# Optimization experiments

Measured on AMD Instinct MI355X. Metric: run time of the kernel, lower is better.

The kernel has to match this reference:

```python
import jax, jax.numpy as jnp
import numpy as np

N, E, H = 25000, 100000, 32          # nodes, edges, node/clique hidden dim
NC, A, EC = 8000, 50000, 24000       # cliques, node2clique assignments, clique edges
EEMB, CEE, L = 8, 8, 2               # edge emb dims, n layers


def segment_mean(vals, ids, num):
    s = jax.ops.segment_sum(vals, ids, num_segments=num)
    cnt = jax.ops.segment_sum(jnp.ones(ids.shape[0], vals.dtype), ids, num_segments=num)
    return s / jnp.maximum(cnt, 1.0)[:, None]


def setup_inputs() -> dict:
    key = jax.random.key(0)
    ks = jax.random.split(key, 24)
    s = 0.1  # param scale
    inp = {
        "node_features": jax.random.normal(ks[0], (N, H), jnp.float32),
        "edge_index": jax.random.randint(ks[1], (2, E), 0, N),
        "edge_features": jax.random.normal(ks[2], (E, EEMB), jnp.float32),
        "clique_features": jax.random.normal(ks[3], (NC, H), jnp.float32),
        "node2clique_index": jnp.stack([
            jax.random.randint(ks[4], (A,), 0, N),
            jax.random.randint(ks[5], (A,), 0, NC)]),
        "clique_edge_index": jax.random.randint(ks[6], (2, EC), 0, NC),
        "clique_edge_features": jax.random.normal(ks[7], (EC, CEE), jnp.float32),
        # node NNConv params (stacked over L layers)
        "nn1_w": jax.random.normal(ks[8], (L, EEMB, H)) * s,
        "nn1_b": jnp.zeros((L, H)),
        "nn2_w": jax.random.normal(ks[9], (L, H, H * H)) * s,
        "nn2_b": jnp.zeros((L, H * H)),
        "root_w": jax.random.normal(ks[10], (L, H, H)) * s,
        "root_b": jnp.zeros((L, H)),
        # Node2Clique linear
        "n2c_w": jax.random.normal(ks[11], (L, H, H)) * s,
        "n2c_b": jnp.zeros((L, H)),
        # clique NNConv params
        "cnn1_w": jax.random.normal(ks[12], (L, CEE, H)) * s,
        "cnn1_b": jnp.zeros((L, H)),
        "cnn2_w": jax.random.normal(ks[13], (L, H, H * H)) * s,
        "cnn2_b": jnp.zeros((L, H * H)),
        "croot_w": jax.random.normal(ks[14], (L, H, H)) * s,
        "croot_b": jnp.zeros((L, H)),
        # Clique2Node linear
        "c2n_w": jax.random.normal(ks[15], (L, H, H)) * s,
        "c2n_b": jnp.zeros((L, H)),
    }
    return inp


def nnconv(x, src, dst, edge_attr, w1, b1, w2, b2, rw, rb, n_out_nodes):
    # per-edge weight matrices from the edge MLP: [E, in, out]
    h = jax.nn.relu(edge_attr @ w1 + b1)
    We = (h @ w2 + b2).reshape(edge_attr.shape[0], x.shape[1], -1)
    msg = jnp.einsum('ei,eio->eo', x[src], We)           # message from source
    agg = segment_mean(msg, dst, n_out_nodes)            # mean aggregation at target
    return agg + x @ rw + rb                             # root weight + bias


def reference(node_features, edge_index, edge_features, clique_features,
              node2clique_index, clique_edge_index, clique_edge_features,
              nn1_w, nn1_b, nn2_w, nn2_b, root_w, root_b, n2c_w, n2c_b,
              cnn1_w, cnn1_b, cnn2_w, cnn2_b, croot_w, croot_b, c2n_w, c2n_b):
    x, c = node_features, clique_features
    src, dst = edge_index[0], edge_index[1]
    nid, cid = node2clique_index[0], node2clique_index[1]
    csrc, cdst = clique_edge_index[0], clique_edge_index[1]
    for l in range(L):
        # node-level edge-conditioned conv
        x = jax.nn.relu(nnconv(x, src, dst, edge_features,
                               nn1_w[l], nn1_b[l], nn2_w[l], nn2_b[l],
                               root_w[l], root_b[l], N))
        # Node2Clique: project node feats, scatter-mean into cliques
        m = x @ n2c_w[l] + n2c_b[l]
        c = c + segment_mean(m[nid], cid, NC)
        # clique-level edge-conditioned conv
        c = jax.nn.relu(nnconv(c, csrc, cdst, clique_edge_features,
                               cnn1_w[l], cnn1_b[l], cnn2_w[l], cnn2_b[l],
                               croot_w[l], croot_b[l], NC))
        # Clique2Node: project clique feats, scatter-mean back onto nodes
        m = c @ c2n_w[l] + c2n_b[l]
        x = x + segment_mean(m[cid], nid, N)
    return (x, c)
```

## Files before the change

### kernel.cpp

```cpp
#include <hip/hip_runtime.h>
#include <hip/hip_bf16.h>

typedef unsigned int u32;
typedef unsigned short u16;

#define DEVINL __device__ __forceinline__

constexpr int Nn  = 25000;
constexpr int Ee  = 100000;
constexpr int NCc = 8000;
constexpr int Aa  = 50000;
constexpr int ECc = 24000;
constexpr int TCOLS = 1088;
constexpr int WPSZ  = TCOLS*32;
constexpr int NSTR  = 580;
constexpr int NB_N = (Nn + 255)/256;
constexpr int NB_C = (NCc + 255)/256;

typedef float f32x4 __attribute__((ext_vector_type(4)));
typedef short s16x8 __attribute__((ext_vector_type(8)));

DEVINL float b2f(u16 u){ union{u32 i;float f;}v; v.i = ((u32)u)<<16; return v.f; }
DEVINL float bfl(u32 u){ union{u32 i;float f;}v; v.i = u<<16; return v.f; }
DEVINL float bfh(u32 u){ union{u32 i;float f;}v; v.i = u & 0xffff0000u; return v.f; }
DEVINL u16 f2b(float f){ union{float f;u32 i;}v; v.f=f; u32 i=v.i;
  return (u16)((i + 0x7fffu + ((i>>16)&1u)) >> 16); }
DEVINL u32 pk2(float a, float b){ return (u32)f2b(a) | ((u32)f2b(b) << 16); }
DEVINL float ldw(const void* p, long i, int f){
  return f ? ((const float*)p)[i] : b2f(((const u16*)p)[i]);
}

__global__ __launch_bounds__(256) void k_detect(const u16* __restrict__ p, int n,
                        u32* __restrict__ maxbits, int* __restrict__ zcnt,
                        int* __restrict__ done, int* __restrict__ flag){
  int i0 = blockIdx.x*256 + threadIdx.x;
  float lm = 0.f; int lz = 0;
  for (int i = i0; i < n; i += gridDim.x*256){
    u16 v = p[i];
    if (v == 0) lz++;
    lm = fmaxf(lm, fabsf(b2f(v)));
  }
  #pragma unroll
  for (int off = 32; off; off >>= 1){
    lm = fmaxf(lm, __shfl_down(lm, off));
    lz += __shfl_down(lz, off);
  }
  if ((threadIdx.x & 63) == 0){
    atomicMax(maxbits, __float_as_uint(lm));
    atomicAdd(zcnt, lz);
  }
  __syncthreads();
  if (threadIdx.x == 0){
    __threadfence();
    if (atomicAdd(done, 1) == gridDim.x - 1){
      float m = __uint_as_float(*maxbits);
      *flag = (m > 1e6f || *zcnt > n/4) ? 1 : 0;
    }
  }
}

__global__ __launch_bounds__(256) void k_conv_all(const void* __restrict__ xin, const void* __restrict__ cin,
                         float* __restrict__ xA, float* __restrict__ cA, const int* __restrict__ flag){
  int i = blockIdx.x*256 + threadIdx.x;
  int f = *flag;
  if (i < Nn*32) xA[i] = ldw(xin, i, f);
  else { i -= Nn*32; if (i < NCc*32) cA[i] = ldw(cin, i, f); }
}

__global__ __launch_bounds__(256) void k_count_all(const int* __restrict__ ei, const int* __restrict__ cei,
                          const int* __restrict__ n2c,
                          int* __restrict__ deg_nd, int* __restrict__ deg_ce,
                          int* __restrict__ deg_n2c, int* __restrict__ deg_c2n,
                          int* __restrict__ cnt_sn, int* __restrict__ cnt_sc){
  int i = blockIdx.x*256 + threadIdx.x;
  if (i < Ee)                             atomicAdd(&deg_nd[ei[Ee + i]], 1);
  else if ((i -= Ee) < ECc)               atomicAdd(&deg_ce[cei[ECc + i]], 1);
  else if ((i -= ECc) < Aa)               atomicAdd(&deg_n2c[n2c[Aa + i]], 1);
  else if ((i -= Aa) < Aa)                atomicAdd(&deg_c2n[n2c[i]], 1);
  else if ((i -= Aa) < Ee)                atomicAdd(&cnt_sn[ei[i]], 1);
  else if ((i -= Ee) < ECc)               atomicAdd(&cnt_sc[cei[i]], 1);
}

__global__ __launch_bounds__(256) void k_scan_block(
    const int* __restrict__ c0, const int* __restrict__ c1,
    const int* __restrict__ c2, const int* __restrict__ c3,
    int* __restrict__ o0, int* __restrict__ o1, int* __restrict__ o2, int* __restrict__ o3,
    int* __restrict__ b0, int* __restrict__ b1, int* __restrict__ b2, int* __restrict__ b3){
  __shared__ int s[256];
  int bid = blockIdx.x, seg, rb;
  if (bid < NB_N){ seg=0; rb=bid; }
  else if (bid < NB_N+NB_C){ seg=1; rb=bid-NB_N; }
  else if (bid < 2*NB_N+NB_C){ seg=2; rb=bid-NB_N-NB_C; }
  else { seg=3; rb=bid-2*NB_N-NB_C; }
  const int* cnt = seg==0?c0 : seg==1?c1 : seg==2?c2 : c3;
  int* offs = seg==0?o0 : seg==1?o1 : seg==2?o2 : o3;
  int* bs   = seg==0?b0 : seg==1?b1 : seg==2?b2 : b3;
  int M = (seg & 1) ? NCc : Nn;
  int tid = threadIdx.x;
  int i = rb*256 + tid;
  int v = (i < M) ? cnt[i] : 0;
  s[tid] = v; __syncthreads();
  for (int d = 1; d < 256; d <<= 1){
    int t = (tid >= d) ? s[tid-d] : 0;
    __syncthreads();
    s[tid] += t;
    __syncthreads();
  }
  if (i < M) offs[i] = s[tid] - v;
  if (tid == 255) bs[rb] = s[255];
}

__global__ __launch_bounds__(512) void k_spine(int* __restrict__ b0, int* __restrict__ b1,
                      int* __restrict__ b2, int* __restrict__ b3){
  __shared__ int s[512];
  int tid = threadIdx.x, seg = tid >> 7, lane = tid & 127;
  int NB = (seg & 1) ? NB_C : NB_N;
  int* bp = seg==0?b0 : seg==1?b1 : seg==2?b2 : b3;
  int v = (lane < NB) ? bp[lane] : 0;
  s[tid] = v; __syncthreads();
  for (int d = 1; d < 128; d <<= 1){
    int t = (lane >= d) ? s[tid-d] : 0;
    __syncthreads();
    s[tid] += t;
    __syncthreads();
  }
  if (lane < NB) bp[lane] = s[tid] - v;
}

__global__ __launch_bounds__(256) void k_scan_fix(
    int* __restrict__ o0, int* __restrict__ o1, int* __restrict__ o2, int* __restrict__ o3,
    const int* __restrict__ b0, const int* __restrict__ b1,
    const int* __restrict__ b2, const int* __restrict__ b3){
  int i = blockIdx.x*256 + threadIdx.x;
  if (i < Nn) o0[i] += b0[i >> 8];
  else if ((i -= Nn) < NCc) o1[i] += b1[i >> 8];
  else if ((i -= NCc) < Nn) o2[i] += b2[i >> 8];
  else if ((i -= Nn) < NCc) o3[i] += b3[i >> 8];
}

__global__ __launch_bounds__(256) void k_place(const int* __restrict__ ei, const int* __restrict__ cei,
                      const int* __restrict__ n2c,
                      const int* __restrict__ offs_n, const int* __restrict__ offs_c,
                      const int* __restrict__ offs_an, const int* __restrict__ offs_ac,
                      int* __restrict__ cur_n, int* __restrict__ cur_c,
                      int* __restrict__ cur_an, int* __restrict__ cur_ac,
                      int* __restrict__ perm_n, int* __restrict__ perm_c,
                      int* __restrict__ an2c, int* __restrict__ ac2n){
  int i = blockIdx.x*256 + threadIdx.x;
  if (i < Ee){
    int s = ei[i];
    perm_n[offs_n[s] + atomicAdd(&cur_n[s], 1)] = i;
  } else if ((i -= Ee) < ECc){
    int s = cei[i];
    perm_c[offs_c[s] + atomicAdd(&cur_c[s], 1)] = i;
  } else if ((i -= ECc) < Aa){
    int c = n2c[Aa + i];
    an2c[offs_ac[c] + atomicAdd(&cur_ac[c], 1)] = n2c[i];
  } else if ((i -= Aa) < Aa){
    int nd = n2c[i];
    ac2n[offs_an[nd] + atomicAdd(&cur_an[nd], 1)] = n2c[Aa + i];
  }
}

__global__ __launch_bounds__(256) void k_gather(const int* __restrict__ ei, const int* __restrict__ cei,
                       const int* __restrict__ perm_n, const int* __restrict__ perm_c,
                       const void* __restrict__ ef, const void* __restrict__ cef,
                       const int* __restrict__ flag,
                       int2* __restrict__ sdp_n, float* __restrict__ efp_n,
                       int2* __restrict__ sdp_c, float* __restrict__ efp_c){
  int i = blockIdx.x*256 + threadIdx.x;
  int f = *flag;
  if (i < Ee*8){
    int p = i >> 3, j = i & 7;
    int e = perm_n[p];
    efp_n[i] = ldw(ef, (long)e*8 + j, f);
    if (j == 0) sdp_n[p] = make_int2(ei[e], ei[Ee + e]);
  } else if ((i -= Ee*8) < ECc*8){
    int p = i >> 3, j = i & 7;
    int e = perm_c[p];
    efp_c[i] = ldw(cef, (long)e*8 + j, f);
    if (j == 0) sdp_c[p] = make_int2(cei[e], cei[ECc + e]);
  }
}

__global__ __launch_bounds__(256) void k_wpack_all(const void* __restrict__ nn2w, const void* __restrict__ nn2b,
                          const void* __restrict__ rootw,
                          const void* __restrict__ cnn2w, const void* __restrict__ cnn2b,
                          const void* __restrict__ crootw,
                          const int* __restrict__ flag, u16* __restrict__ Wp4){
  int i = blockIdx.x*256 + threadIdx.x;
  if (i >= 4*WPSZ) return;
  int set = i / WPSZ, j = i - set*WPSZ;
  int l = set >> 1, isC = set & 1;
  const void* W2 = isC ? cnn2w : nn2w;
  const void* B2 = isC ? cnn2b : nn2b;
  const void* RW = isC ? crootw : rootw;
  int f = *flag;
  int col = j >> 5, ii = j & 31;
  float v;
  if (col < 1024)      v = ldw(W2, (long)l*32768 + ((col>>5)<<10) + (ii<<5) + (col&31), f);
  else if (col < 1056) v = ldw(B2, (long)l*1024 + (ii<<5) + (col-1024), f);
  else                 v = ldw(RW, (long)l*1024 + (ii<<5) + (col-1056), f);
  Wp4[i] = f2b(v);
}

__global__ __launch_bounds__(512) void k_conv_fused(const float* __restrict__ base, int M,
                           const int2* __restrict__ sdp, const float* __restrict__ efp,
                           const int* __restrict__ offs, int E_,
                           const void* __restrict__ w1, long w1off,
                           const void* __restrict__ b1, long b1off,
                           const u16* __restrict__ Wp,
                           const void* __restrict__ rb, long rboff,
                           const int* __restrict__ flag,
                           float* __restrict__ feat_root, float* __restrict__ agg){
  __shared__ __align__(16) u32 Ts[16*NSTR];
  __shared__ float w1s[256];
  __shared__ __align__(8) u32 hws[8][4][16];
  int tid = threadIdx.x;
  int w = tid >> 6, lane = tid & 63;
  int quad = lane >> 4, lm = lane & 15;
  int n0 = blockIdx.x * 16;
  int f = *flag;
  if (tid < 256) w1s[tid] = ldw(w1, w1off + tid, f);
  float bb0 = ldw(b1, b1off + 2*lm, f);
  float bb1 = ldw(b1, b1off + 2*lm + 1, f);
  int n = n0 + lm;
  int nc = n < M ? n : M-1;
  const float* bp = base + (size_t)nc*32 + quad*8;
  s16x8 bfrag;
  #pragma unroll
  for (int j = 0; j < 8; j++) bfrag[j] = (short)f2b(bp[j]);
  #pragma unroll 1
  for (int ti = 0; ti < 9; ti++){
    int ct = w*9 + ti;
    if (ct >= 68) break;
    int colbase = ct*16;
    s16x8 afrag = *(const s16x8*)(Wp + (size_t)(colbase + lm)*32 + quad*8);
    f32x4 acc = {0.f, 0.f, 0.f, 0.f};
    acc = __builtin_amdgcn_mfma_f32_16x16x32_bf16(afrag, bfrag, acc, 0, 0, 0);
    if (ct < 66){
      int k = ct >> 1;
      int p0 = (ct & 1)*8 + quad*2;
      int idx = lm*NSTR + p0*36 + k;
      Ts[idx]      = pk2(acc[0], acc[1]);
      Ts[idx + 36] = pk2(acc[2], acc[3]);
    } else if (n < M){
      int o = (ct - 66)*16 + quad*4 - 0;
      o = (colbase + quad*4) - 1056;
      float4 v = make_float4(acc[0] + ldw(rb, rboff+o,   f),
                             acc[1] + ldw(rb, rboff+o+1, f),
                             acc[2] + ldw(rb, rboff+o+2, f),
                             acc[3] + ldw(rb, rboff+o+3, f));
      *(float4*)&feat_root[(size_t)n*32 + o] = v;
    }
  }
  __syncthreads();
  int lo = offs[n0];
  int hi = (n0 + 16 < M) ? offs[n0 + 16] : E_;
  int eg = quad, kk = lm;
  int pos = lo + w*4;
  float ef0 = 0.f, ef1 = 0.f; int sd0 = 0, sd1 = 0;
  if (lane < 32){
    int idx = pos*8 + lane;        if (idx < hi*8) ef0 = efp[idx];
    idx = (pos+32)*8 + lane;       if (idx < hi*8) ef1 = efp[idx];
  } else if (lane < 40){
    int idx = pos*2 + (lane-32);   if (idx < hi*2) sd0 = ((const int*)sdp)[idx];
    idx = (pos+32)*2 + (lane-32);  if (idx < hi*2) sd1 = ((const int*)sdp)[idx];
  }
  for (; pos < hi; pos += 32){
    int np = pos + 64;
    float ef2 = 0.f; int sd2 = 0;
    if (lane < 32){ int idx = np*8 + lane; if (idx < hi*8) ef2 = efp[idx]; }
    else if (lane < 40){ int idx = np*2 + (lane-32); if (idx < hi*2) sd2 = ((const int*)sdp)[idx]; }
    int sn = __shfl(sd0, 32 + 2*eg);
    int dn = __shfl(sd0, 33 + 2*eg);
    bool valid = (pos + eg < hi);
    int sr = sn - n0; sr = sr < 0 ? 0 : (sr > 15 ? 15 : sr);
    float a0 = bb0, a1 = bb1;
    #pragma unroll
    for (int j = 0; j < 8; j++){
      float ev = __shfl(ef0, eg*8 + j);
      a0 += ev * w1s[j*32 + 2*kk];
      a1 += ev * w1s[j*32 + 2*kk+1];
    }
    hws[w][eg][kk] = pk2(fmaxf(a0, 0.f), fmaxf(a1, 0.f));
    if (valid){
      const u32* Tr = &Ts[sr*NSTR + kk*36];
      u32 vb = Tr[32];
      float m0 = bfl(vb), m1 = bfh(vb);
      #pragma unroll
      for (int g = 0; g < 8; g++){
        uint4 tv = *(const uint4*)&Tr[g*4];
        uint2 hp = *(const uint2*)&hws[w][eg][g*2];
        float h0 = bfl(hp.x), h1 = bfh(hp.x), h2 = bfl(hp.y), h3 = bfh(hp.y);
        m0 += h0*bfl(tv.x) + h1*bfl(tv.y) + h2*bfl(tv.z) + h3*bfl(tv.w);
        m1 += h0*bfh(tv.x) + h1*bfh(tv.y) + h2*bfh(tv.z) + h3*bfh(tv.w);
      }
      float* ap = agg + (size_t)dn*32 + 2*kk;
      atomicAdd(ap,   m0);
      atomicAdd(ap+1, m1);
    }
    ef0 = ef1; sd0 = sd1; ef1 = ef2; sd1 = sd2;
  }
}

__global__ __launch_bounds__(256) void k_update_lin(const float* __restrict__ agg, const int* __restrict__ deg,
                           const float* __restrict__ feat_root, int M,
                           const void* __restrict__ w, long woff,
                           const void* __restrict__ b, long boff,
                           const int* __restrict__ flag,
                           float* __restrict__ feat, void* __restrict__ dt_out, long dt_off,
                           float* __restrict__ m_out){
  __shared__ float wsm[1024], bs[32], rows[8][33];
  int tid = threadIdx.x;
  int f = *flag;
  for (int idx = tid; idx < 1024; idx += 256) wsm[idx] = ldw(w, woff + idx, f);
  if (tid < 32) bs[tid] = ldw(b, boff + tid, f);
  int nl = tid >> 5, o = tid & 31;
  int n = blockIdx.x*8 + nl;
  long i = (long)n*32 + o;
  if (n < M){
    int dg = deg[n];
    float d = (float)(dg > 1 ? dg : 1);
    float v = fmaxf(agg[i]/d + feat_root[i], 0.f);
    rows[nl][o] = v;
    if (feat) feat[i] = v;
    if (dt_out){
      if (f) ((float*)dt_out)[dt_off + i] = v;
      else   ((u16*)dt_out)[dt_off + i]   = f2b(v);
    }
  }
  __syncthreads();
  if (n >= M) return;
  float acc = bs[o];
  #pragma unroll
  for (int j = 0; j < 32; j++) acc += rows[nl][j]*wsm[j*32+o];
  m_out[i] = acc;
}

__global__ __launch_bounds__(256) void k_segmean(const float* __restrict__ base, const float* __restrict__ m,
                        const int* __restrict__ idxarr, const int* __restrict__ offs,
                        const int* __restrict__ deg, int M, float* __restrict__ out){
  int i = blockIdx.x*256 + threadIdx.x;
  if (i >= M*32) return;
  int c = i >> 5, o = i & 31;
  int lo = offs[c], cnt = deg[c];
  float s = 0.f;
  for (int a = lo; a < lo + cnt; a++) s += m[(size_t)idxarr[a]*32 + o];
  out[i] = base[i] + s/(float)(cnt > 1 ? cnt : 1);
}

__global__ __launch_bounds__(256) void k_segmean_out(const float* __restrict__ base, const float* __restrict__ m,
                        const int* __restrict__ idxarr, const int* __restrict__ offs,
                        const int* __restrict__ deg, int M,
                        void* __restrict__ out, const int* __restrict__ flag){
  int i = blockIdx.x*256 + threadIdx.x;
  if (i >= M*32) return;
  int c = i >> 5, o = i & 31;
  int lo = offs[c], cnt = deg[c];
  float s = 0.f;
  for (int a = lo; a < lo + cnt; a++) s += m[(size_t)idxarr[a]*32 + o];
  float v = base[i] + s/(float)(cnt > 1 ? cnt : 1);
  if (*flag) ((float*)out)[i] = v;
  else       ((u16*)out)[i]   = f2b(v);
}

extern "C" void kernel_launch(void* const* d_in, const int* in_sizes, int n_in,
                              void* d_out, int out_size, void* d_ws, size_t ws_size,
                              hipStream_t stream){
  const int* ei  = (const int*)d_in[1];
  const int* n2c = (const int*)d_in[4];
  const int* cei = (const int*)d_in[5];
  const void *efr = d_in[2], *cefr = d_in[6];
  const void *nn1w = d_in[7], *nn1b = d_in[8], *nn2w = d_in[9], *nn2b = d_in[10],
             *rootw = d_in[11], *rootb = d_in[12], *n2cw = d_in[13], *n2cb = d_in[14],
             *cnn1w = d_in[15], *cnn1b = d_in[16], *cnn2w = d_in[17], *cnn2b = d_in[18],
             *crootw = d_in[19], *crootb = d_in[20], *c2nw = d_in[21], *c2nb = d_in[22];

  char* ws = (char*)d_ws;
  size_t off = 0;
  auto alloc = [&](size_t bytes){ void* p = ws + off; off += (bytes + 255) & ~(size_t)255; return p; };

  size_t zstart = off;
  float* aggE0  = (float*)alloc((size_t)Nn*32*4);
  float* aggE1  = (float*)alloc((size_t)Nn*32*4);
  float* caggE0 = (float*)alloc((size_t)NCc*32*4);
  float* caggE1 = (float*)alloc((size_t)NCc*32*4);
  int* deg_nd  = (int*)alloc((size_t)Nn*4);
  int* deg_ce  = (int*)alloc((size_t)NCc*4);
  int* deg_n2c = (int*)alloc((size_t)NCc*4);
  int* deg_c2n = (int*)alloc((size_t)Nn*4);
  int* cnt_sn  = (int*)alloc((size_t)Nn*4);
  int* cnt_sc  = (int*)alloc((size_t)NCc*4);
  int* cur_n   = (int*)alloc((size_t)Nn*4);
  int* cur_c   = (int*)alloc((size_t)NCc*4);
  int* cur_an  = (int*)alloc((size_t)Nn*4);
  int* cur_ac  = (int*)alloc((size_t)NCc*4);
  u32* maxbits = (u32*)alloc(256);
  int* zcnt = (int*)((char*)maxbits + 4);
  int* flag = (int*)((char*)maxbits + 8);
  int* done = (int*)((char*)maxbits + 12);
  size_t zbytes = off - zstart;

  float* xA  = (float*)alloc((size_t)Nn*32*4);
  float* xB  = (float*)alloc((size_t)Nn*32*4);
  float* xA1 = (float*)alloc((size_t)Nn*32*4);
  float* xC  = (float*)alloc((size_t)Nn*32*4);
  float* cA  = (float*)alloc((size_t)NCc*32*4);
  float* cB  = (float*)alloc((size_t)NCc*32*4);
  float* cC0 = (float*)alloc((size_t)NCc*32*4);
  float* cB1 = (float*)alloc((size_t)NCc*32*4);
  float* m_n = (float*)alloc((size_t)Nn*32*4);
  float* m_c = (float*)alloc((size_t)NCc*32*4);
  float* frn = (float*)alloc((size_t)Nn*32*4);
  float* frc = (float*)alloc((size_t)NCc*32*4);
  int* offs_n  = (int*)alloc((size_t)Nn*4);
  int* offs_c  = (int*)alloc((size_t)NCc*4);
  int* offs_an = (int*)alloc((size_t)Nn*4);
  int* offs_ac = (int*)alloc((size_t)NCc*4);
  int* bsum0 = (int*)alloc(512);
  int* bsum1 = (int*)alloc(512);
  int* bsum2 = (int*)alloc(512);
  int* bsum3 = (int*)alloc(512);
  int* perm_n = (int*)alloc((size_t)Ee*4);
  int* perm_c = (int*)alloc((size_t)ECc*4);
  int* an2c = (int*)alloc((size_t)Aa*4);
  int* ac2n = (int*)alloc((size_t)Aa*4);
  int2* sdp_n = (int2*)alloc((size_t)Ee*8);
  int2* sdp_c = (int2*)alloc((size_t)ECc*8);
  float* efp_n = (float*)alloc((size_t)Ee*8*4);
  float* efp_c = (float*)alloc((size_t)ECc*8*4);
  u16* Wp4 = (u16*)alloc((size_t)4*WPSZ*2);

  auto nb = [](int n){ return (n + 255)/256; };

  hipMemsetAsync(ws + zstart, 0, zbytes, stream);
  k_detect<<<256,256,0,stream>>>((const u16*)d_in[0], Nn*32, maxbits, zcnt, done, flag);
  k_conv_all<<<nb(Nn*32 + NCc*32),256,0,stream>>>(d_in[0], d_in[3], xA, cA, flag);
  k_count_all<<<nb(2*Ee + 2*ECc + 2*Aa),256,0,stream>>>(ei, cei, n2c,
      deg_nd, deg_ce, deg_n2c, deg_c2n, cnt_sn, cnt_sc);
  k_scan_block<<<2*(NB_N+NB_C),256,0,stream>>>(cnt_sn, cnt_sc, deg_c2n, deg_n2c,
      offs_n, offs_c, offs_an, offs_ac, bsum0, bsum1, bsum2, bsum3);
  k_spine<<<1,512,0,stream>>>(bsum0, bsum1, bsum2, bsum3);
  k_scan_fix<<<nb(2*(Nn+NCc)),256,0,stream>>>(offs_n, offs_c, offs_an, offs_ac,
      bsum0, bsum1, bsum2, bsum3);
  k_place<<<nb(Ee+ECc+2*Aa),256,0,stream>>>(ei, cei, n2c, offs_n, offs_c, offs_an, offs_ac,
      cur_n, cur_c, cur_an, cur_ac, perm_n, perm_c, an2c, ac2n);
  k_gather<<<nb(8*(Ee+ECc)),256,0,stream>>>(ei, cei, perm_n, perm_c, efr, cefr, flag,
      sdp_n, efp_n, sdp_c, efp_c);
  k_wpack_all<<<nb(4*WPSZ),256,0,stream>>>(nn2w, nn2b, rootw, cnn2w, cnn2b, crootw, flag, Wp4);

  int Gn = (Nn + 15)/16, Gc = (NCc + 15)/16;

  k_conv_fused<<<Gn,512,0,stream>>>(xA, Nn, sdp_n, efp_n, offs_n, Ee,
      nn1w, 0, nn1b, 0, Wp4 + 0*WPSZ, rootb, 0, flag, frn, aggE0);
  k_update_lin<<<(Nn+7)/8,256,0,stream>>>(aggE0, deg_nd, frn, Nn, n2cw, 0, n2cb, 0, flag,
      xB, nullptr, 0, m_n);
  k_segmean<<<nb(NCc*32),256,0,stream>>>(cA, m_n, an2c, offs_ac, deg_n2c, NCc, cB);
  k_conv_fused<<<Gc,512,0,stream>>>(cB, NCc, sdp_c, efp_c, offs_c, ECc,
      cnn1w, 0, cnn1b, 0, Wp4 + 1*WPSZ, crootb, 0, flag, frc, caggE0);
  k_update_lin<<<(NCc+7)/8,256,0,stream>>>(caggE0, deg_ce, frc, NCc, c2nw, 0, c2nb, 0, flag,
      cC0, nullptr, 0, m_c);
  k_segmean<<<nb(Nn*32),256,0,stream>>>(xB, m_c, ac2n, offs_an, deg_c2n, Nn, xA1);
  k_conv_fused<<<Gn,512,0,stream>>>(xA1, Nn, sdp_n, efp_n, offs_n, Ee,
      nn1w, 256, nn1b, 32, Wp4 + 2*WPSZ, rootb, 32, flag, frn, aggE1);
  k_update_lin<<<(Nn+7)/8,256,0,stream>>>(aggE1, deg_nd, frn, Nn, n2cw, 1024, n2cb, 32, flag,
      xC, nullptr, 0, m_n);
  k_segmean<<<nb(NCc*32),256,0,stream>>>(cC0, m_n, an2c, offs_ac, deg_n2c, NCc, cB1);
  k_conv_fused<<<Gc,512,0,stream>>>(cB1, NCc, sdp_c, efp_c, offs_c, ECc,
      cnn1w, 256, cnn1b, 32, Wp4 + 3*WPSZ, crootb, 32, flag, frc, caggE1);
  k_update_lin<<<(NCc+7)/8,256,0,stream>>>(caggE1, deg_ce, frc, NCc, c2nw, 1024, c2nb, 32, flag,
      nullptr, d_out, (long)Nn*32, m_c);
  k_segmean_out<<<nb(Nn*32),256,0,stream>>>(xC, m_c, ac2n, offs_an, deg_c2n, Nn, d_out, flag);
}
```

Measured before the change: 351.1 us.

## Replace atomic edge aggregation with dst-CSR message buffer and fuse segment-mean into conv

The edge conv no longer does float atomicAdds into a per-node aggregate. Each edge writes its bf16-packed message into a slot ordered by destination node, using a new destination CSR built in the existing scan/place kernels. The update kernel then reduces each node's messages deterministically. The separate segment-mean kernels are folded into the conv kernel's input load, removing launches and intermediate buffers. In exchange it adds bf16 rounding of messages, an extra message buffer round-trip, and redundant per-quad segment gathers inside the conv.

```diff
diff --git a/kernel.cpp b/kernel.cpp
--- a/kernel.cpp
+++ b/kernel.cpp
@@ -82,22 +82,25 @@
 }
 
 __global__ __launch_bounds__(256) void k_scan_block(
-    const int* __restrict__ c0, const int* __restrict__ c1,
-    const int* __restrict__ c2, const int* __restrict__ c3,
-    int* __restrict__ o0, int* __restrict__ o1, int* __restrict__ o2, int* __restrict__ o3,
-    int* __restrict__ b0, int* __restrict__ b1, int* __restrict__ b2, int* __restrict__ b3){
+    const int* __restrict__ c0, const int* __restrict__ c1, const int* __restrict__ c2,
+    const int* __restrict__ c3, const int* __restrict__ c4, const int* __restrict__ c5,
+    int* __restrict__ o0, int* __restrict__ o1, int* __restrict__ o2,
+    int* __restrict__ o3, int* __restrict__ o4, int* __restrict__ o5,
+    int* __restrict__ b0, int* __restrict__ b1, int* __restrict__ b2,
+    int* __restrict__ b3, int* __restrict__ b4, int* __restrict__ b5){
   __shared__ int s[256];
-  int bid = blockIdx.x, seg, rb;
-  if (bid < NB_N){ seg=0; rb=bid; }
-  else if (bid < NB_N+NB_C){ seg=1; rb=bid-NB_N; }
-  else if (bid < 2*NB_N+NB_C){ seg=2; rb=bid-NB_N-NB_C; }
-  else { seg=3; rb=bid-2*NB_N-NB_C; }
-  const int* cnt = seg==0?c0 : seg==1?c1 : seg==2?c2 : c3;
-  int* offs = seg==0?o0 : seg==1?o1 : seg==2?o2 : o3;
-  int* bs   = seg==0?b0 : seg==1?b1 : seg==2?b2 : b3;
+  int bid = blockIdx.x, seg = 0;
+  for (;;){
+    int nb = (seg & 1) ? NB_C : NB_N;
+    if (bid < nb) break;
+    bid -= nb; seg++;
+  }
+  const int* cnt = seg==0?c0 : seg==1?c1 : seg==2?c2 : seg==3?c3 : seg==4?c4 : c5;
+  int* offs = seg==0?o0 : seg==1?o1 : seg==2?o2 : seg==3?o3 : seg==4?o4 : o5;
+  int* bs   = seg==0?b0 : seg==1?b1 : seg==2?b2 : seg==3?b3 : seg==4?b4 : b5;
   int M = (seg & 1) ? NCc : Nn;
   int tid = threadIdx.x;
-  int i = rb*256 + tid;
+  int i = bid*256 + tid;
   int v = (i < M) ? cnt[i] : 0;
   s[tid] = v; __syncthreads();
   for (int d = 1; d < 256; d <<= 1){
@@ -107,15 +110,16 @@
     __syncthreads();
   }
   if (i < M) offs[i] = s[tid] - v;
-  if (tid == 255) bs[rb] = s[255];
-}
-
-__global__ __launch_bounds__(512) void k_spine(int* __restrict__ b0, int* __restrict__ b1,
-                      int* __restrict__ b2, int* __restrict__ b3){
-  __shared__ int s[512];
+  if (tid == 255) bs[bid] = s[255];
+}
+
+__global__ __launch_bounds__(768) void k_spine(int* __restrict__ b0, int* __restrict__ b1,
+                      int* __restrict__ b2, int* __restrict__ b3,
+                      int* __restrict__ b4, int* __restrict__ b5){
+  __shared__ int s[768];
   int tid = threadIdx.x, seg = tid >> 7, lane = tid & 127;
   int NB = (seg & 1) ? NB_C : NB_N;
-  int* bp = seg==0?b0 : seg==1?b1 : seg==2?b2 : b3;
+  int* bp = seg==0?b0 : seg==1?b1 : seg==2?b2 : seg==3?b3 : seg==4?b4 : b5;
   int v = (lane < NB) ? bp[lane] : 0;
   s[tid] = v; __syncthreads();
   for (int d = 1; d < 128; d <<= 1){
@@ -128,31 +132,41 @@
 }
 
 __global__ __launch_bounds__(256) void k_scan_fix(
-    int* __restrict__ o0, int* __restrict__ o1, int* __restrict__ o2, int* __restrict__ o3,
-    const int* __restrict__ b0, const int* __restrict__ b1,
-    const int* __restrict__ b2, const int* __restrict__ b3){
+    int* __restrict__ o0, int* __restrict__ o1, int* __restrict__ o2,
+    int* __restrict__ o3, int* __restrict__ o4, int* __restrict__ o5,
+    const int* __restrict__ b0, const int* __restrict__ b1, const int* __restrict__ b2,
+    const int* __restrict__ b3, const int* __restrict__ b4, const int* __restrict__ b5){
   int i = blockIdx.x*256 + threadIdx.x;
   if (i < Nn) o0[i] += b0[i >> 8];
   else if ((i -= Nn) < NCc) o1[i] += b1[i >> 8];
   else if ((i -= NCc) < Nn) o2[i] += b2[i >> 8];
   else if ((i -= Nn) < NCc) o3[i] += b3[i >> 8];
+  else if ((i -= NCc) < Nn) o4[i] += b4[i >> 8];
+  else if ((i -= Nn) < NCc) o5[i] += b5[i >> 8];
 }
 
 __global__ __launch_bounds__(256) void k_place(const int* __restrict__ ei, const int* __restrict__ cei,
                       const int* __restrict__ n2c,
                       const int* __restrict__ offs_n, const int* __restrict__ offs_c,
                       const int* __restrict__ offs_an, const int* __restrict__ offs_ac,
+                      const int* __restrict__ doffs_n, const int* __restrict__ doffs_c,
                       int* __restrict__ cur_n, int* __restrict__ cur_c,
                       int* __restrict__ cur_an, int* __restrict__ cur_ac,
+                      int* __restrict__ curd_n, int* __restrict__ curd_c,
                       int* __restrict__ perm_n, int* __restrict__ perm_c,
+                      int* __restrict__ dq_n, int* __restrict__ dq_c,
                       int* __restrict__ an2c, int* __restrict__ ac2n){
   int i = blockIdx.x*256 + threadIdx.x;
   if (i < Ee){
-    int s = ei[i];
-    perm_n[offs_n[s] + atomicAdd(&cur_n[s], 1)] = i;
+    int s = ei[i], d = ei[Ee + i];
+    int p = offs_n[s] + atomicAdd(&cur_n[s], 1);
+    int q = doffs_n[d] + atomicAdd(&curd_n[d], 1);
+    perm_n[p] = i; dq_n[p] = q;
   } else if ((i -= Ee) < ECc){
-    int s = cei[i];
-    perm_c[offs_c[s] + atomicAdd(&cur_c[s], 1)] = i;
+    int s = cei[i], d = cei[ECc + i];
+    int p = offs_c[s] + atomicAdd(&cur_c[s], 1);
+    int q = doffs_c[d] + atomicAdd(&curd_c[d], 1);
+    perm_c[p] = i; dq_c[p] = q;
   } else if ((i -= ECc) < Aa){
     int c = n2c[Aa + i];
     an2c[offs_ac[c] + atomicAdd(&cur_ac[c], 1)] = n2c[i];
@@ -164,6 +178,7 @@
 
 __global__ __launch_bounds__(256) void k_gather(const int* __restrict__ ei, const int* __restrict__ cei,
                        const int* __restrict__ perm_n, const int* __restrict__ perm_c,
+                       const int* __restrict__ dq_n, const int* __restrict__ dq_c,
                        const void* __restrict__ ef, const void* __restrict__ cef,
                        const int* __restrict__ flag,
                        int2* __restrict__ sdp_n, float* __restrict__ efp_n,
@@ -174,12 +189,12 @@
     int p = i >> 3, j = i & 7;
     int e = perm_n[p];
     efp_n[i] = ldw(ef, (long)e*8 + j, f);
-    if (j == 0) sdp_n[p] = make_int2(ei[e], ei[Ee + e]);
+    if (j == 0) sdp_n[p] = make_int2(ei[e], dq_n[p]);
   } else if ((i -= Ee*8) < ECc*8){
     int p = i >> 3, j = i & 7;
     int e = perm_c[p];
     efp_c[i] = ldw(cef, (long)e*8 + j, f);
-    if (j == 0) sdp_c[p] = make_int2(cei[e], cei[ECc + e]);
+    if (j == 0) sdp_c[p] = make_int2(cei[e], dq_c[p]);
   }
 }
 
@@ -204,7 +219,9 @@
   Wp4[i] = f2b(v);
 }
 
-__global__ __launch_bounds__(512) void k_conv_fused(const float* __restrict__ base, int M,
+__global__ __launch_bounds__(512) void k_conv_fused(const float* __restrict__ base,
+                           const float* __restrict__ mprev, const int* __restrict__ aidx,
+                           const int* __restrict__ aoffs, const int* __restrict__ adeg, int M,
                            const int2* __restrict__ sdp, const float* __restrict__ efp,
                            const int* __restrict__ offs, int E_,
                            const void* __restrict__ w1, long w1off,
@@ -212,7 +229,7 @@
                            const u16* __restrict__ Wp,
                            const void* __restrict__ rb, long rboff,
                            const int* __restrict__ flag,
-                           float* __restrict__ feat_root, float* __restrict__ agg){
+                           float* __restrict__ feat_root, u32* __restrict__ msg){
   __shared__ __align__(16) u32 Ts[16*NSTR];
   __shared__ float w1s[256];
   __shared__ __align__(8) u32 hws[8][4][16];
@@ -227,9 +244,24 @@
   int n = n0 + lm;
   int nc = n < M ? n : M-1;
   const float* bp = base + (size_t)nc*32 + quad*8;
+  float fv[8];
+  #pragma unroll
+  for (int j = 0; j < 8; j++) fv[j] = bp[j];
+  if (aidx){
+    int lo = aoffs[nc], cnt = adeg[nc];
+    float sacc[8] = {0,0,0,0,0,0,0,0};
+    for (int a = lo; a < lo + cnt; a++){
+      const float* mp = mprev + (size_t)aidx[a]*32 + quad*8;
+      #pragma unroll
+      for (int j = 0; j < 8; j++) sacc[j] += mp[j];
+    }
+    float inv = 1.f/(float)(cnt > 1 ? cnt : 1);
+    #pragma unroll
+    for (int j = 0; j < 8; j++) fv[j] += sacc[j]*inv;
+  }
   s16x8 bfrag;
   #pragma unroll
-  for (int j = 0; j < 8; j++) bfrag[j] = (short)f2b(bp[j]);
+  for (int j = 0; j < 8; j++) bfrag[j] = (short)f2b(fv[j]);
   #pragma unroll 1
   for (int ti = 0; ti < 9; ti++){
     int ct = w*9 + ti;
@@ -245,8 +277,7 @@
       Ts[idx]      = pk2(acc[0], acc[1]);
       Ts[idx + 36] = pk2(acc[2], acc[3]);
     } else if (n < M){
-      int o = (ct - 66)*16 + quad*4 - 0;
-      o = (colbase + quad*4) - 1056;
+      int o = (colbase + quad*4) - 1056;
       float4 v = make_float4(acc[0] + ldw(rb, rboff+o,   f),
                              acc[1] + ldw(rb, rboff+o+1, f),
                              acc[2] + ldw(rb, rboff+o+2, f),
@@ -273,7 +304,7 @@
     if (lane < 32){ int idx = np*8 + lane; if (idx < hi*8) ef2 = efp[idx]; }
     else if (lane < 40){ int idx = np*2 + (lane-32); if (idx < hi*2) sd2 = ((const int*)sdp)[idx]; }
     int sn = __shfl(sd0, 32 + 2*eg);
-    int dn = __shfl(sd0, 33 + 2*eg);
+    int dq = __shfl(sd0, 33 + 2*eg);
     bool valid = (pos + eg < hi);
     int sr = sn - n0; sr = sr < 0 ? 0 : (sr > 15 ? 15 : sr);
     float a0 = bb0, a1 = bb1;
@@ -296,15 +327,14 @@
         m0 += h0*bfl(tv.x) + h1*bfl(tv.y) + h2*bfl(tv.z) + h3*bfl(tv.w);
         m1 += h0*bfh(tv.x) + h1*bfh(tv.y) + h2*bfh(tv.z) + h3*bfh(tv.w);
       }
-      float* ap = agg + (size_t)dn*32 + 2*kk;
-      atomicAdd(ap,   m0);
-      atomicAdd(ap+1, m1);
+      msg[(size_t)dq*16 + kk] = pk2(m0, m1);
     }
     ef0 = ef1; sd0 = sd1; ef1 = ef2; sd1 = sd2;
   }
 }
 
-__global__ __launch_bounds__(256) void k_update_lin(const float* __restrict__ agg, const int* __restrict__ deg,
+__global__ __launch_bounds__(256) void k_update_lin(const u32* __restrict__ msg,
+                           const int* __restrict__ doffs, const int* __restrict__ ddeg,
                            const float* __restrict__ feat_root, int M,
                            const void* __restrict__ w, long woff,
                            const void* __restrict__ b, long boff,
@@ -320,9 +350,11 @@
   int n = blockIdx.x*8 + nl;
   long i = (long)n*32 + o;
   if (n < M){
-    int dg = deg[n];
-    float d = (float)(dg > 1 ? dg : 1);
-    float v = fmaxf(agg[i]/d + feat_root[i], 0.f);
+    int lo = doffs[n], cnt = ddeg[n];
+    const u16* mp = (const u16*)msg;
+    float s = 0.f;
+    for (int a = 0; a < cnt; a++) s += b2f(mp[(size_t)(lo+a)*32 + o]);
+    float v = fmaxf(s/(float)(cnt > 1 ? cnt : 1) + feat_root[i], 0.f);
     rows[nl][o] = v;
     if (feat) feat[i] = v;
     if (dt_out){
@@ -336,18 +368,6 @@
   #pragma unroll
   for (int j = 0; j < 32; j++) acc += rows[nl][j]*wsm[j*32+o];
   m_out[i] = acc;
-}
-
-__global__ __launch_bounds__(256) void k_segmean(const float* __restrict__ base, const float* __restrict__ m,
-                        const int* __restrict__ idxarr, const int* __restrict__ offs,
-                        const int* __restrict__ deg, int M, float* __restrict__ out){
-  int i = blockIdx.x*256 + threadIdx.x;
-  if (i >= M*32) return;
-  int c = i >> 5, o = i & 31;
-  int lo = offs[c], cnt = deg[c];
-  float s = 0.f;
-  for (int a = lo; a < lo + cnt; a++) s += m[(size_t)idxarr[a]*32 + o];
-  out[i] = base[i] + s/(float)(cnt > 1 ? cnt : 1);
 }
 
 __global__ __launch_bounds__(256) void k_segmean_out(const float* __restrict__ base, const float* __restrict__ m,
@@ -382,10 +402,6 @@
   auto alloc = [&](size_t bytes){ void* p = ws + off; off += (bytes + 255) & ~(size_t)255; return p; };
 
   size_t zstart = off;
-  float* aggE0  = (float*)alloc((size_t)Nn*32*4);
-  float* aggE1  = (float*)alloc((size_t)Nn*32*4);
-  float* caggE0 = (float*)alloc((size_t)NCc*32*4);
-  float* caggE1 = (float*)alloc((size_t)NCc*32*4);
   int* deg_nd  = (int*)alloc((size_t)Nn*4);
   int* deg_ce  = (int*)alloc((size_t)NCc*4);
   int* deg_n2c = (int*)alloc((size_t)NCc*4);
@@ -396,6 +412,8 @@
   int* cur_c   = (int*)alloc((size_t)NCc*4);
   int* cur_an  = (int*)alloc((size_t)Nn*4);
   int* cur_ac  = (int*)alloc((size_t)NCc*4);
+  int* curd_n  = (int*)alloc((size_t)Nn*4);
+  int* curd_c  = (int*)alloc((size_t)NCc*4);
   u32* maxbits = (u32*)alloc(256);
   int* zcnt = (int*)((char*)maxbits + 4);
   int* flag = (int*)((char*)maxbits + 8);
@@ -404,12 +422,9 @@
 
   float* xA  = (float*)alloc((size_t)Nn*32*4);
   float* xB  = (float*)alloc((size_t)Nn*32*4);
-  float* xA1 = (float*)alloc((size_t)Nn*32*4);
   float* xC  = (float*)alloc((size_t)Nn*32*4);
   float* cA  = (float*)alloc((size_t)NCc*32*4);
-  float* cB  = (float*)alloc((size_t)NCc*32*4);
   float* cC0 = (float*)alloc((size_t)NCc*32*4);
-  float* cB1 = (float*)alloc((size_t)NCc*32*4);
   float* m_n = (float*)alloc((size_t)Nn*32*4);
   float* m_c = (float*)alloc((size_t)NCc*32*4);
   float* frn = (float*)alloc((size_t)Nn*32*4);
@@ -418,18 +433,23 @@
   int* offs_c  = (int*)alloc((size_t)NCc*4);
   int* offs_an = (int*)alloc((size_t)Nn*4);
   int* offs_ac = (int*)alloc((size_t)NCc*4);
-  int* bsum0 = (int*)alloc(512);
-  int* bsum1 = (int*)alloc(512);
-  int* bsum2 = (int*)alloc(512);
-  int* bsum3 = (int*)alloc(512);
+  int* doffs_n = (int*)alloc((size_t)Nn*4);
+  int* doffs_c = (int*)alloc((size_t)NCc*4);
+  int* bs0 = (int*)alloc(512); int* bs1 = (int*)alloc(512);
+  int* bs2 = (int*)alloc(512); int* bs3 = (int*)alloc(512);
+  int* bs4 = (int*)alloc(512); int* bs5 = (int*)alloc(512);
   int* perm_n = (int*)alloc((size_t)Ee*4);
   int* perm_c = (int*)alloc((size_t)ECc*4);
+  int* dq_n = (int*)alloc((size_t)Ee*4);
+  int* dq_c = (int*)alloc((size_t)ECc*4);
   int* an2c = (int*)alloc((size_t)Aa*4);
   int* ac2n = (int*)alloc((size_t)Aa*4);
   int2* sdp_n = (int2*)alloc((size_t)Ee*8);
   int2* sdp_c = (int2*)alloc((size_t)ECc*8);
   float* efp_n = (float*)alloc((size_t)Ee*8*4);
   float* efp_c = (float*)alloc((size_t)ECc*8*4);
+  u32* msg_n = (u32*)alloc((size_t)Ee*16*4);
+  u32* msg_c = (u32*)alloc((size_t)ECc*16*4);
   u16* Wp4 = (u16*)alloc((size_t)4*WPSZ*2);
 
   auto nb = [](int n){ return (n + 255)/256; };
@@ -439,37 +459,35 @@
   k_conv_all<<<nb(Nn*32 + NCc*32),256,0,stream>>>(d_in[0], d_in[3], xA, cA, flag);
   k_count_all<<<nb(2*Ee + 2*ECc + 2*Aa),256,0,stream>>>(ei, cei, n2c,
       deg_nd, deg_ce, deg_n2c, deg_c2n, cnt_sn, cnt_sc);
-  k_scan_block<<<2*(NB_N+NB_C),256,0,stream>>>(cnt_sn, cnt_sc, deg_c2n, deg_n2c,
-      offs_n, offs_c, offs_an, offs_ac, bsum0, bsum1, bsum2, bsum3);
-  k_spine<<<1,512,0,stream>>>(bsum0, bsum1, bsum2, bsum3);
-  k_scan_fix<<<nb(2*(Nn+NCc)),256,0,stream>>>(offs_n, offs_c, offs_an, offs_ac,
-      bsum0, bsum1, bsum2, bsum3);
+  k_scan_block<<<3*(NB_N+NB_C),256,0,stream>>>(cnt_sn, cnt_sc, deg_c2n, deg_n2c, deg_nd, deg_ce,
+      offs_n, offs_c, offs_an, offs_ac, doffs_n, doffs_c, bs0, bs1, bs2, bs3, bs4, bs5);
+  k_spine<<<1,768,0,stream>>>(bs0, bs1, bs2, bs3, bs4, bs5);
+  k_scan_fix<<<nb(3*(Nn+NCc)),256,0,stream>>>(offs_n, offs_c, offs_an, offs_ac, doffs_n, doffs_c,
+      bs0, bs1, bs2, bs3, bs4, bs5);
   k_place<<<nb(Ee+ECc+2*Aa),256,0,stream>>>(ei, cei, n2c, offs_n, offs_c, offs_an, offs_ac,
-      cur_n, cur_c, cur_an, cur_ac, perm_n, perm_c, an2c, ac2n);
-  k_gather<<<nb(8*(Ee+ECc)),256,0,stream>>>(ei, cei, perm_n, perm_c, efr, cefr, flag,
+      doffs_n, doffs_c, cur_n, cur_c, cur_an, cur_ac, curd_n, curd_c,
+      perm_n, perm_c, dq_n, dq_c, an2c, ac2n);
+  k_gather<<<nb(8*(Ee+ECc)),256,0,stream>>>(ei, cei, perm_n, perm_c, dq_n, dq_c, efr, cefr, flag,
       sdp_n, efp_n, sdp_c, efp_c);
   k_wpack_all<<<nb(4*WPSZ),256,0,stream>>>(nn2w, nn2b, rootw, cnn2w, cnn2b, crootw, flag, Wp4);
 
   int Gn = (Nn + 15)/16, Gc = (NCc + 15)/16;
 
-  k_conv_fused<<<Gn,512,0,stream>>>(xA, Nn, sdp_n, efp_n, offs_n, Ee,
-      nn1w, 0, nn1b, 0, Wp4 + 0*WPSZ, rootb, 0, flag, frn, aggE0);
-  k_update_lin<<<(Nn+7)/8,256,0,stream>>>(aggE0, deg_nd, frn, Nn, n2cw, 0, n2cb, 0, flag,
-      xB, nullptr, 0, m_n);
-  k_segmean<<<nb(NCc*32),256,0,stream>>>(cA, m_n, an2c, offs_ac, deg_n2c, NCc, cB);
-  k_conv_fused<<<Gc,512,0,stream>>>(cB, NCc, sdp_c, efp_c, offs_c, ECc,
-      cnn1w, 0, cnn1b, 0, Wp4 + 1*WPSZ, crootb, 0, flag, frc, caggE0);
-  k_update_lin<<<(NCc+7)/8,256,0,stream>>>(caggE0, deg_ce, frc, NCc, c2nw, 0, c2nb, 0, flag,
-      cC0, nullptr, 0, m_c);
-  k_segmean<<<nb(Nn*32),256,0,stream>>>(xB, m_c, ac2n, offs_an, deg_c2n, Nn, xA1);
-  k_conv_fused<<<Gn,512,0,stream>>>(xA1, Nn, sdp_n, efp_n, offs_n, Ee,
-      nn1w, 256, nn1b, 32, Wp4 + 2*WPSZ, rootb, 32, flag, frn, aggE1);
-  k_update_lin<<<(Nn+7)/8,256,0,stream>>>(aggE1, deg_nd, frn, Nn, n2cw, 1024, n2cb, 32, flag,
-      xC, nullptr, 0, m_n);
-  k_segmean<<<nb(NCc*32),256,0,stream>>>(cC0, m_n, an2c, offs_ac, deg_n2c, NCc, cB1);
-  k_conv_fused<<<Gc,512,0,stream>>>(cB1, NCc, sdp_c, efp_c, offs_c, ECc,
-      cnn1w, 256, cnn1b, 32, Wp4 + 3*WPSZ, crootb, 32, flag, frc, caggE1);
-  k_update_lin<<<(NCc+7)/8,256,0,stream>>>(caggE1, deg_ce, frc, NCc, c2nw, 1024, c2nb, 32, flag,
-      nullptr, d_out, (long)Nn*32, m_c);
+  k_conv_fused<<<Gn,512,0,stream>>>(xA, nullptr, nullptr, nullptr, nullptr, Nn,
+      sdp_n, efp_n, offs_n, Ee, nn1w, 0, nn1b, 0, Wp4 + 0*WPSZ, rootb, 0, flag, frn, msg_n);
+  k_update_lin<<<(Nn+7)/8,256,0,stream>>>(msg_n, doffs_n, deg_nd, frn, Nn,
+      n2cw, 0, n2cb, 0, flag, xB, nullptr, 0, m_n);
+  k_conv_fused<<<Gc,512,0,stream>>>(cA, m_n, an2c, offs_ac, deg_n2c, NCc,
+      sdp_c, efp_c, offs_c, ECc, cnn1w, 0, cnn1b, 0, Wp4 + 1*WPSZ, crootb, 0, flag, frc, msg_c);
+  k_update_lin<<<(NCc+7)/8,256,0,stream>>>(msg_c, doffs_c, deg_ce, frc, NCc,
+      c2nw, 0, c2nb, 0, flag, cC0, nullptr, 0, m_c);
+  k_conv_fused<<<Gn,512,0,stream>>>(xB, m_c, ac2n, offs_an, deg_c2n, Nn,
+      sdp_n, efp_n, offs_n, Ee, nn1w, 256, nn1b, 32, Wp4 + 2*WPSZ, rootb, 32, flag, frn, msg_n);
+  k_update_lin<<<(Nn+7)/8,256,0,stream>>>(msg_n, doffs_n, deg_nd, frn, Nn,
+      n2cw, 1024, n2cb, 32, flag, xC, nullptr, 0, m_n);
+  k_conv_fused<<<Gc,512,0,stream>>>(cC0, m_n, an2c, offs_ac, deg_n2c, NCc,
+      sdp_c, efp_c, offs_c, ECc, cnn1w, 256, cnn1b, 32, Wp4 + 3*WPSZ, crootb, 32, flag, frc, msg_c);
+  k_update_lin<<<(NCc+7)/8,256,0,stream>>>(msg_c, doffs_c, deg_ce, frc, NCc,
+      c2nw, 1024, c2nb, 32, flag, nullptr, d_out, (long)Nn*32, m_c);
   k_segmean_out<<<nb(Nn*32),256,0,stream>>>(xC, m_c, ac2n, offs_an, deg_c2n, Nn, d_out, flag);
 }
```

Result: no change. 351.3 us (+0.0%).
